# Kernel tuning notes

Measured on AMD Instinct MI355X. Metric: run time of the kernel, lower is better.

Reference implementation:

```python
import jax, jax.numpy as jnp
import numpy as np

ALPHA = 0.2  # leaky-relu negative slope AND the residual scale self.alpha

def setup_inputs() -> dict:
    key = jax.random.key(0)
    k1, k2, k3 = jax.random.split(key, 3)
    B, N, C_in, C_out = 8, 2048, 128, 128
    text = jax.random.normal(k1, (B, N, C_in), dtype=jnp.float32)
    adj = jnp.ones((B, N, N), dtype=jnp.float32)  # unused by the layer's forward
    W = jax.random.normal(k2, (C_in, C_out), dtype=jnp.float32) * (1.414 / np.sqrt(C_in + C_out))
    a = jax.random.normal(k3, (2 * C_out, 1), dtype=jnp.float32) * (1.414 / np.sqrt(2 * C_out + 1))
    return {"text": text, "adj": adj, "W": W, "a": a}

def reference(text, adj, W, a):
    # text: [B,N,C_in]; adj is unused (faithful to the source forward).
    h = jnp.einsum('bnc,cf->bnf', text, W)                  # [B,N,F]
    F_out = W.shape[1]
    a1 = a[:F_out, 0]                                       # score contribution of node i
    a2 = a[F_out:, 0]                                       # score contribution of node j
    s1 = jnp.einsum('bnf,f->bn', h, a1)                     # [B,N]
    s2 = jnp.einsum('bnf,f->bn', h, a2)                     # [B,N]
    # leakyrelu(cat(h_i,h_j) @ a) == leakyrelu(s1_i + s2_j): avoids O(N^2*2F) concat
    e = jax.nn.leaky_relu(s1[:, :, None] + s2[:, None, :], negative_slope=ALPHA)  # [B,N,N]
    attention = jax.nn.softmax(e, axis=2)                   # dropout is a no-op in eval mode
    h_prime = jnp.einsum('bij,bjf->bif', attention, h)      # [B,N,F]
    return jax.nn.elu(h_prime + ALPHA * h)
```

## Files before the change

### kernel.cpp

```cpp
#include <hip/hip_runtime.h>
#include <math.h>

#define LRELU_ALPHA 0.2f

constexpr int B_ = 8;
constexpr int N_ = 2048;
constexpr int M_ = B_ * N_;
constexpr int SEG = 32;
constexpr int NSEG = N_ / SEG;

__global__ __launch_bounds__(512) void k_gemm(const float* __restrict__ text,
                                              const float* __restrict__ W,
                                              const float* __restrict__ a,
                                              float* __restrict__ h,
                                              float* __restrict__ s1,
                                              float* __restrict__ s2,
                                              float* __restrict__ eN0,
                                              float* __restrict__ eP0) {
    __shared__ float As[64 * 33];
    __shared__ float Ws[32 * 128];
    const int tid = threadIdx.x;
    const int r0  = blockIdx.x * 64;
    const int cx  = tid & 15;
    const int ry  = tid >> 4;
    const int c0  = cx * 8;
    const int rr0 = ry * 2;

    float acc[2][8];
#pragma unroll
    for (int i = 0; i < 2; ++i)
#pragma unroll
        for (int j = 0; j < 8; ++j) acc[i][j] = 0.f;

    for (int kk = 0; kk < 128; kk += 32) {
        for (int idx = tid; idx < 64 * 32; idx += 512) {
            int r = idx >> 5, c = idx & 31;
            As[r * 33 + c] = text[(r0 + r) * 128 + kk + c];
        }
        for (int idx = tid; idx < 32 * 128; idx += 512) {
            int k = idx >> 7, f = idx & 127;
            Ws[k * 128 + f] = W[(kk + k) * 128 + f];
        }
        __syncthreads();
#pragma unroll
        for (int k = 0; k < 32; ++k) {
            float4 w0 = *(const float4*)&Ws[k * 128 + c0];
            float4 w1 = *(const float4*)&Ws[k * 128 + c0 + 4];
#pragma unroll
            for (int i = 0; i < 2; ++i) {
                float av = As[(rr0 + i) * 33 + k];
                acc[i][0] += av * w0.x; acc[i][1] += av * w0.y;
                acc[i][2] += av * w0.z; acc[i][3] += av * w0.w;
                acc[i][4] += av * w1.x; acc[i][5] += av * w1.y;
                acc[i][6] += av * w1.z; acc[i][7] += av * w1.w;
            }
        }
        __syncthreads();
    }

    float4 a10 = *(const float4*)&a[c0];
    float4 a11 = *(const float4*)&a[c0 + 4];
    float4 a20 = *(const float4*)&a[128 + c0];
    float4 a21 = *(const float4*)&a[128 + c0 + 4];

#pragma unroll
    for (int i = 0; i < 2; ++i) {
        int row = r0 + rr0 + i;
        float4 o0 = {acc[i][0], acc[i][1], acc[i][2], acc[i][3]};
        float4 o1 = {acc[i][4], acc[i][5], acc[i][6], acc[i][7]};
        *(float4*)&h[row * 128 + c0]     = o0;
        *(float4*)&h[row * 128 + c0 + 4] = o1;

        float p1 = o0.x * a10.x + o0.y * a10.y + o0.z * a10.z + o0.w * a10.w
                 + o1.x * a11.x + o1.y * a11.y + o1.z * a11.z + o1.w * a11.w;
        float p2 = o0.x * a20.x + o0.y * a20.y + o0.z * a20.z + o0.w * a20.w
                 + o1.x * a21.x + o1.y * a21.y + o1.z * a21.z + o1.w * a21.w;
#pragma unroll
        for (int off = 8; off >= 1; off >>= 1) {
            p1 += __shfl_xor(p1, off);
            p2 += __shfl_xor(p2, off);
        }
        if (cx == 0) {
            s1[row] = p1;
            s2[row] = p2;
            eN0[row] = expf(LRELU_ALPHA * p2);
            eP0[row] = expf(p2);
        }
    }
}

__global__ __launch_bounds__(512) void k_rank(const float* __restrict__ s2,
                                              const float* __restrict__ eN0,
                                              const float* __restrict__ eP0,
                                              const float* __restrict__ s1,
                                              int* __restrict__ perm,
                                              float* __restrict__ eNs,
                                              float* __restrict__ ePs,
                                              int* __restrict__ rank,
                                              float* __restrict__ ZN,
                                              float* __restrict__ ZP) {
    __shared__ float ls2[2048], leN[2048], leP[2048];
    __shared__ int   redc[512], redm[512];
    __shared__ float redn[512], redp[512];

    const int b  = blockIdx.x >> 5;
    const int eb = blockIdx.x & 31;
    const int tid = threadIdx.x;
    const int e = tid & 63;
    const int c = tid >> 6;

    {
        const float4* g2 = (const float4*)(s2  + b * 2048);
        const float4* gn = (const float4*)(eN0 + b * 2048);
        const float4* gp = (const float4*)(eP0 + b * 2048);
        ((float4*)ls2)[tid] = g2[tid];
        ((float4*)leN)[tid] = gn[tid];
        ((float4*)leP)[tid] = gp[tid];
    }
    __syncthreads();

    const int i  = eb * 64 + e;
    const int gi = b * 2048 + i;
    const float myS2 = ls2[i];
    const float thr  = -s1[gi];

    int cnt = 0, mr = 0;
    float sn = 0.f, sp = 0.f;
    const int j0 = c * 256;
#pragma unroll 4
    for (int j = j0; j < j0 + 256; j += 4) {
        float4 v  = *(const float4*)&ls2[j];
        float4 en = *(const float4*)&leN[j];
        float4 ep = *(const float4*)&leP[j];
#define PROC(vv, ee, pp, jj)                                             \
        { bool le = (vv) <= thr;                                         \
          cnt += le ? 1 : 0;                                             \
          sn  += le ? (ee) : 0.f;                                        \
          sp  += le ? 0.f : (pp);                                        \
          mr  += ((vv) < myS2 || ((vv) == myS2 && (jj) < i)) ? 1 : 0; }
        PROC(v.x, en.x, ep.x, j + 0)
        PROC(v.y, en.y, ep.y, j + 1)
        PROC(v.z, en.z, ep.z, j + 2)
        PROC(v.w, en.w, ep.w, j + 3)
#undef PROC
    }
    redc[tid] = cnt; redm[tid] = mr; redn[tid] = sn; redp[tid] = sp;
    __syncthreads();
    if (c == 0) {
        int tc = 0, tm = 0; float tn = 0.f, tp = 0.f;
#pragma unroll
        for (int cc = 0; cc < 8; ++cc) {
            tc += redc[cc * 64 + e];
            tm += redm[cc * 64 + e];
            tn += redn[cc * 64 + e];
            tp += redp[cc * 64 + e];
        }
        perm[b * 2048 + tm] = i;
        eNs [b * 2048 + tm] = leN[i];
        ePs [b * 2048 + tm] = leP[i];
        rank[gi] = tc;
        ZN[gi] = tn;
        ZP[gi] = tp;
    }
}

__global__ __launch_bounds__(128) void k_segsum(const float* __restrict__ h,
                                                const int* __restrict__ perm,
                                                const float* __restrict__ eNs,
                                                const float* __restrict__ ePs,
                                                float* __restrict__ segN,
                                                float* __restrict__ segP) {
    const int blk = blockIdx.x;
    const int b = blk >> 6, s = blk & 63;
    const int f = threadIdx.x;
    const int rbase = s * SEG;
    float an = 0.f, ap = 0.f;
#pragma unroll 4
    for (int r = 0; r < SEG; ++r) {
        int rr = b * 2048 + rbase + r;
        float hv = h[(b * 2048 + perm[rr]) * 128 + f];
        an += eNs[rr] * hv;
        ap += ePs[rr] * hv;
    }
    segN[blk * 128 + f] = an;
    segP[blk * 128 + f] = ap;
}

__global__ __launch_bounds__(128) void k_prefix(const float* __restrict__ h,
                                                const int* __restrict__ perm,
                                                const float* __restrict__ eNs,
                                                const float* __restrict__ ePs,
                                                const float* __restrict__ segN,
                                                const float* __restrict__ segP,
                                                float* __restrict__ Pre,
                                                float* __restrict__ Suf) {
    const int blk = blockIdx.x;
    const int b = blk >> 6, s = blk & 63;
    const int f = threadIdx.x;
    const int rbase = s * SEG;

    float an = 0.f, ap = 0.f;
    for (int ss = 0; ss < s; ++ss)        an += segN[(b * NSEG + ss) * 128 + f];
    for (int ss = s + 1; ss < NSEG; ++ss) ap += segP[(b * NSEG + ss) * 128 + f];

    float hv[SEG];
#pragma unroll
    for (int r = 0; r < SEG; ++r) {
        int rr = b * 2048 + rbase + r;
        hv[r] = h[(b * 2048 + perm[rr]) * 128 + f];
        Pre[(b * 2049 + rbase + r) * 128 + f] = an;
        an += eNs[rr] * hv[r];
    }
#pragma unroll
    for (int r = SEG - 1; r >= 0; --r) {
        int rr = b * 2048 + rbase + r;
        ap += ePs[rr] * hv[r];
        Suf[(b * 2049 + rbase + r) * 128 + f] = ap;
    }
    if (s == NSEG - 1) {
        Pre[(b * 2049 + 2048) * 128 + f] = an;
        Suf[(b * 2049 + 2048) * 128 + f] = 0.f;
    }
}

__global__ __launch_bounds__(256) void k_out(const float* __restrict__ h,
                                             const float* __restrict__ s1,
                                             const int* __restrict__ rank,
                                             const float* __restrict__ ZN,
                                             const float* __restrict__ ZP,
                                             const float* __restrict__ Pre,
                                             const float* __restrict__ Suf,
                                             float* __restrict__ out) {
    const int tid = threadIdx.x;
    const int lr = tid >> 7, f = tid & 127;
    const int i = blockIdx.x * 2 + lr;
    const int b = i >> 11;

    const float s1v = s1[i];
    const float E1 = expf(s1v);
    const float E2 = expf(LRELU_ALPHA * s1v);
    const int   r  = rank[i];
    const float Z  = E1 * ZP[i] + E2 * ZN[i];
    const int o = (b * 2049 + r) * 128 + f;
    const float hp = (E1 * Suf[o] + E2 * Pre[o]) / Z;
    const float x = hp + LRELU_ALPHA * h[i * 128 + f];
    out[i * 128 + f] = (x > 0.f) ? x : expm1f(x);
}

extern "C" void kernel_launch(void* const* d_in, const int* in_sizes, int n_in,
                              void* d_out, int out_size, void* d_ws, size_t ws_size,
                              hipStream_t stream) {
    const float* text = (const float*)d_in[0];
    const float* W = (const float*)d_in[2];
    const float* a = (const float*)d_in[3];
    float* out = (float*)d_out;

    float* p = (float*)d_ws;
    float* h    = p; p += (size_t)M_ * 128;
    float* s1   = p; p += M_;
    float* s2   = p; p += M_;
    float* eN0  = p; p += M_;
    float* eP0  = p; p += M_;
    int*   perm = (int*)p; p += M_;
    float* eNs  = p; p += M_;
    float* ePs  = p; p += M_;
    int*   rank = (int*)p; p += M_;
    float* ZN   = p; p += M_;
    float* ZP   = p; p += M_;
    float* segN = p; p += B_ * NSEG * 128;
    float* segP = p; p += B_ * NSEG * 128;
    float* Pre  = p; p += (size_t)B_ * 2049 * 128;
    float* Suf  = p; p += (size_t)B_ * 2049 * 128;

    hipLaunchKernelGGL(k_gemm,   dim3(M_ / 64),   dim3(512), 0, stream,
                       text, W, a, h, s1, s2, eN0, eP0);
    hipLaunchKernelGGL(k_rank,   dim3(B_ * 32),   dim3(512), 0, stream,
                       s2, eN0, eP0, s1, perm, eNs, ePs, rank, ZN, ZP);
    hipLaunchKernelGGL(k_segsum, dim3(B_ * NSEG), dim3(128), 0, stream,
                       h, perm, eNs, ePs, segN, segP);
    hipLaunchKernelGGL(k_prefix, dim3(B_ * NSEG), dim3(128), 0, stream,
                       h, perm, eNs, ePs, segN, segP, Pre, Suf);
    hipLaunchKernelGGL(k_out,    dim3(M_ / 2),    dim3(256), 0, stream,
                       h, s1, rank, ZN, ZP, Pre, Suf, out);
}
```

Baseline: 238.8 us.

## Fuse prefix scan and output into one kernel with shared-memory prefixes

Replaces the global Pre/Suf prefix arrays and separate output kernel with a fused kernel that keeps per-segment prefix/suffix sums in shared memory. k_rank now buckets each query row by its rank segment via atomic counters, so each fused block processes only the queries landing in its segment. This removes large global writes and reads of the prefix arrays and one launch, but adds atomics and serial per-block query loops whose load depends on the rank distribution.

Measured after the change: 257.3 us. 7.8% more time.

```diff
diff --git a/kernel.cpp b/kernel.cpp
--- a/kernel.cpp
+++ b/kernel.cpp
@@ -98,7 +98,9 @@
                                               float* __restrict__ ePs,
                                               int* __restrict__ rank,
                                               float* __restrict__ ZN,
-                                              float* __restrict__ ZP) {
+                                              float* __restrict__ ZP,
+                                              int* __restrict__ qcnt,
+                                              int* __restrict__ qlist) {
     __shared__ float ls2[2048], leN[2048], leP[2048];
     __shared__ int   redc[512], redm[512];
     __shared__ float redn[512], redp[512];
@@ -161,6 +163,9 @@
         rank[gi] = tc;
         ZN[gi] = tn;
         ZP[gi] = tp;
+        int sq = tc >> 5; if (sq > NSEG - 1) sq = NSEG - 1;
+        int slot = atomicAdd(&qcnt[b * NSEG + sq], 1);
+        qlist[(b * NSEG + sq) * 2048 + slot] = i;
     }
 }
 
@@ -186,65 +191,63 @@
     segP[blk * 128 + f] = ap;
 }
 
-__global__ __launch_bounds__(128) void k_prefix(const float* __restrict__ h,
-                                                const int* __restrict__ perm,
-                                                const float* __restrict__ eNs,
-                                                const float* __restrict__ ePs,
-                                                const float* __restrict__ segN,
-                                                const float* __restrict__ segP,
-                                                float* __restrict__ Pre,
-                                                float* __restrict__ Suf) {
+__global__ __launch_bounds__(128) void k_fused(const float* __restrict__ h,
+                                               const int* __restrict__ perm,
+                                               const float* __restrict__ eNs,
+                                               const float* __restrict__ ePs,
+                                               const float* __restrict__ segN,
+                                               const float* __restrict__ segP,
+                                               const int* __restrict__ qcnt,
+                                               const int* __restrict__ qlist,
+                                               const int* __restrict__ rank,
+                                               const float* __restrict__ s1,
+                                               const float* __restrict__ ZN,
+                                               const float* __restrict__ ZP,
+                                               float* __restrict__ out) {
+    __shared__ float PreL[33 * 128];
+    __shared__ float SufL[33 * 128];
     const int blk = blockIdx.x;
     const int b = blk >> 6, s = blk & 63;
     const int f = threadIdx.x;
-    const int rbase = s * SEG;
-
-    float an = 0.f, ap = 0.f;
-    for (int ss = 0; ss < s; ++ss)        an += segN[(b * NSEG + ss) * 128 + f];
-    for (int ss = s + 1; ss < NSEG; ++ss) ap += segP[(b * NSEG + ss) * 128 + f];
+
+    float cn = 0.f, cp = 0.f;
+    for (int ss = 0; ss < s; ++ss)         cn += segN[(b * NSEG + ss) * 128 + f];
+    for (int ss = s + 1; ss < NSEG; ++ss)  cp += segP[(b * NSEG + ss) * 128 + f];
 
     float hv[SEG];
-#pragma unroll
-    for (int r = 0; r < SEG; ++r) {
-        int rr = b * 2048 + rbase + r;
-        hv[r] = h[(b * 2048 + perm[rr]) * 128 + f];
-        Pre[(b * 2049 + rbase + r) * 128 + f] = an;
-        an += eNs[rr] * hv[r];
-    }
-#pragma unroll
-    for (int r = SEG - 1; r >= 0; --r) {
-        int rr = b * 2048 + rbase + r;
-        ap += ePs[rr] * hv[r];
-        Suf[(b * 2049 + rbase + r) * 128 + f] = ap;
-    }
-    if (s == NSEG - 1) {
-        Pre[(b * 2049 + 2048) * 128 + f] = an;
-        Suf[(b * 2049 + 2048) * 128 + f] = 0.f;
-    }
-}
-
-__global__ __launch_bounds__(256) void k_out(const float* __restrict__ h,
-                                             const float* __restrict__ s1,
-                                             const int* __restrict__ rank,
-                                             const float* __restrict__ ZN,
-                                             const float* __restrict__ ZP,
-                                             const float* __restrict__ Pre,
-                                             const float* __restrict__ Suf,
-                                             float* __restrict__ out) {
-    const int tid = threadIdx.x;
-    const int lr = tid >> 7, f = tid & 127;
-    const int i = blockIdx.x * 2 + lr;
-    const int b = i >> 11;
-
-    const float s1v = s1[i];
-    const float E1 = expf(s1v);
-    const float E2 = expf(LRELU_ALPHA * s1v);
-    const int   r  = rank[i];
-    const float Z  = E1 * ZP[i] + E2 * ZN[i];
-    const int o = (b * 2049 + r) * 128 + f;
-    const float hp = (E1 * Suf[o] + E2 * Pre[o]) / Z;
-    const float x = hp + LRELU_ALPHA * h[i * 128 + f];
-    out[i * 128 + f] = (x > 0.f) ? x : expm1f(x);
+    float an = 0.f;
+#pragma unroll
+    for (int l = 0; l < SEG; ++l) {
+        int rr = b * 2048 + s * SEG + l;
+        hv[l] = h[(b * 2048 + perm[rr]) * 128 + f];
+        PreL[l * 128 + f] = an;
+        an += eNs[rr] * hv[l];
+    }
+    float ap = 0.f;
+#pragma unroll
+    for (int l = SEG - 1; l >= 0; --l) {
+        int rr = b * 2048 + s * SEG + l;
+        ap += ePs[rr] * hv[l];
+        SufL[l * 128 + f] = ap;
+    }
+    PreL[SEG * 128 + f] = an;
+    SufL[SEG * 128 + f] = 0.f;
+    __syncthreads();
+
+    const int nq = qcnt[b * NSEG + s];
+    const int qbase = (b * NSEG + s) * 2048;
+    for (int k = 0; k < nq; ++k) {
+        int q  = qlist[qbase + k];
+        int gq = b * 2048 + q;
+        float s1v = s1[gq];
+        float E1 = expf(s1v), E2 = expf(LRELU_ALPHA * s1v);
+        float Z = E1 * ZP[gq] + E2 * ZN[gq];
+        int l = rank[gq] - s * SEG;
+        float PreAt = cn + PreL[l * 128 + f];
+        float SufAt = cp + SufL[l * 128 + f];
+        float x = (E1 * SufAt + E2 * PreAt) / Z + LRELU_ALPHA * h[gq * 128 + f];
+        out[gq * 128 + f] = (x > 0.f) ? x : expm1f(x);
+    }
 }
 
 extern "C" void kernel_launch(void* const* d_in, const int* in_sizes, int n_in,
@@ -269,17 +272,16 @@
     float* ZP   = p; p += M_;
     float* segN = p; p += B_ * NSEG * 128;
     float* segP = p; p += B_ * NSEG * 128;
-    float* Pre  = p; p += (size_t)B_ * 2049 * 128;
-    float* Suf  = p; p += (size_t)B_ * 2049 * 128;
-
+    int*   qcnt = (int*)p; p += B_ * NSEG;
+    int*   qlist = (int*)p; p += (size_t)B_ * NSEG * 2048;
+
+    hipMemsetAsync(qcnt, 0, B_ * NSEG * sizeof(int), stream);
     hipLaunchKernelGGL(k_gemm,   dim3(M_ / 64),   dim3(512), 0, stream,
                        text, W, a, h, s1, s2, eN0, eP0);
     hipLaunchKernelGGL(k_rank,   dim3(B_ * 32),   dim3(512), 0, stream,
-                       s2, eN0, eP0, s1, perm, eNs, ePs, rank, ZN, ZP);
+                       s2, eN0, eP0, s1, perm, eNs, ePs, rank, ZN, ZP, qcnt, qlist);
     hipLaunchKernelGGL(k_segsum, dim3(B_ * NSEG), dim3(128), 0, stream,
                        h, perm, eNs, ePs, segN, segP);
-    hipLaunchKernelGGL(k_prefix, dim3(B_ * NSEG), dim3(128), 0, stream,
-                       h, perm, eNs, ePs, segN, segP, Pre, Suf);
-    hipLaunchKernelGGL(k_out,    dim3(M_ / 2),    dim3(256), 0, stream,
-                       h, s1, rank, ZN, ZP, Pre, Suf, out);
-}
+    hipLaunchKernelGGL(k_fused,  dim3(B_ * NSEG), dim3(128), 0, stream,
+                       h, perm, eNs, ePs, segN, segP, qcnt, qlist, rank, s1, ZN, ZP, out);
+}
```
